# Kernel tuning notes

Measured on AMD Instinct MI355X. Metric: run time of the kernel, lower is better.

The kernel has to match this reference:

```python
import jax, jax.numpy as jnp
import numpy as np
import math

E = 512
W = 16


def overlap_and_add(signal, frame_step):
    """signal: [..., frames, frame_length] -> [..., frame_step*(frames-1)+frame_length]."""
    outer = signal.shape[:-2]
    frames, frame_length = signal.shape[-2:]
    subframe_length = math.gcd(frame_length, frame_step)
    subframe_step = frame_step // subframe_length
    subframes_per_frame = frame_length // subframe_length
    output_size = frame_step * (frames - 1) + frame_length
    output_subframes = output_size // subframe_length

    # [B, frames*subframes_per_frame, subframe_length]
    B = int(np.prod(outer)) if outer else 1
    sub = signal.reshape(B, frames * subframes_per_frame, subframe_length)
    # destination subframe index for each source subframe
    idx = (jnp.arange(frames)[:, None] * subframe_step
           + jnp.arange(subframes_per_frame)[None, :]).reshape(-1)
    out = jnp.zeros((B, output_subframes, subframe_length), signal.dtype)
    out = out.at[:, idx, :].add(sub)
    return out.reshape(*outer, output_size)


def setup_inputs() -> dict:
    key = jax.random.key(0)
    k1, k2 = jax.random.split(key)
    mixture_w = jax.random.normal(k1, (8, 2, 16000, E), dtype=jnp.float32)
    # nn.Linear(E, W).weight has shape [W, E]
    basis_weight = jax.random.normal(k2, (W, E), dtype=jnp.float32) * (1.0 / math.sqrt(E))
    return {"mixture_w": mixture_w, "basis_weight": basis_weight}


def reference(mixture_w, basis_weight):
    # est_source: [..., frames, W]
    est_source = jnp.einsum('bckE,wE->bckw', mixture_w, basis_weight)
    return overlap_and_add(est_source, W // 2)
```

## Files before the change

### kernel.cpp

```cpp
#include <hip/hip_runtime.h>


#define FRAMES 16000
#define EDIM   512
#define OUTF   16001
#define OUT_PER_BC 128008
#define BATCHES 16
#define OFPW    128

__global__ __launch_bounds__(128, 2)
void decoder_kernel(const float* __restrict__ A,
                    const float* __restrict__ B,
                    float* __restrict__ out)
{
    const int t   = threadIdx.x;
    const int wid = t >> 6;
    const int l   = t & 63;
    const int wq  = l & 7;
    const int ksl = l >> 3;
    const int bc  = blockIdx.y;
    const int o0  = (blockIdx.x * 2 + wid) * OFPW;

    __shared__ float ring[2][16][16];

    const float4* B4 = (const float4*)B;
    float4 Bw[2][2][8];
    #pragma unroll
    for (int w = 0; w < 2; ++w)
        #pragma unroll
        for (int h = 0; h < 2; ++h)
            #pragma unroll
            for (int j = 0; j < 8; ++j)
                Bw[w][h][j] = B4[(2*wq + w) * 128 + ksl*16 + h*8 + j];

    const float4* Abc = (const float4*)(A + (size_t)bc * FRAMES * EDIM);

    float4 Abuf[2][8];

    auto loadHalf = [&](float4* dst, int f, int h) {
        int fc = f; if (fc < 0) fc = 0; if (fc >= FRAMES) fc = FRAMES - 1;
        const float4* p = Abc + (size_t)fc * 128 + ksl*16 + h*8;
        #pragma unroll
        for (int j = 0; j < 8; ++j) dst[j] = p[j];
    };

    auto processFrame = [&](int f) {
        loadHalf(Abuf[1], f, 1);
        float acc[2][2] = {{0.f,0.f},{0.f,0.f}};
        #pragma unroll
        for (int j = 0; j < 8; ++j) {
            const float4 a = Abuf[0][j];
            acc[0][0] = fmaf(a.x, Bw[0][0][j].x, acc[0][0]);
            acc[0][0] = fmaf(a.y, Bw[0][0][j].y, acc[0][0]);
            acc[0][0] = fmaf(a.z, Bw[0][0][j].z, acc[0][0]);
            acc[0][0] = fmaf(a.w, Bw[0][0][j].w, acc[0][0]);
            acc[1][0] = fmaf(a.x, Bw[1][0][j].x, acc[1][0]);
            acc[1][0] = fmaf(a.y, Bw[1][0][j].y, acc[1][0]);
            acc[1][0] = fmaf(a.z, Bw[1][0][j].z, acc[1][0]);
            acc[1][0] = fmaf(a.w, Bw[1][0][j].w, acc[1][0]);
        }
        loadHalf(Abuf[0], f + 1, 0);
        #pragma unroll
        for (int j = 0; j < 8; ++j) {
            const float4 a = Abuf[1][j];
            acc[0][1] = fmaf(a.x, Bw[0][1][j].x, acc[0][1]);
            acc[0][1] = fmaf(a.y, Bw[0][1][j].y, acc[0][1]);
            acc[0][1] = fmaf(a.z, Bw[0][1][j].z, acc[0][1]);
            acc[0][1] = fmaf(a.w, Bw[0][1][j].w, acc[0][1]);
            acc[1][1] = fmaf(a.x, Bw[1][1][j].x, acc[1][1]);
            acc[1][1] = fmaf(a.y, Bw[1][1][j].y, acc[1][1]);
            acc[1][1] = fmaf(a.z, Bw[1][1][j].z, acc[1][1]);
            acc[1][1] = fmaf(a.w, Bw[1][1][j].w, acc[1][1]);
        }
        float r0 = acc[0][0] + acc[0][1];
        float r1 = acc[1][0] + acc[1][1];
        r0 += __shfl_xor(r0, 8);   r1 += __shfl_xor(r1, 8);
        r0 += __shfl_xor(r0, 16);  r1 += __shfl_xor(r1, 16);
        r0 += __shfl_xor(r0, 32);  r1 += __shfl_xor(r1, 32);
        if (f < 0 || f >= FRAMES) { r0 = 0.f; r1 = 0.f; }
        if (ksl == 0) {
            *(float2*)&ring[wid][f & 15][2*wq] = make_float2(r0, r1);
        }
    };

    loadHalf(Abuf[0], o0 - 1, 0);
    processFrame(o0 - 1);

    for (int b = 0; b < BATCHES; ++b) {
        const int cf = o0 + b * 8;
        #pragma unroll
        for (int r = 0; r < 8; ++r) processFrame(cf + r);
        __syncthreads();
        const int fr = cf + (l >> 3);
        const float v = ring[wid][fr & 15][l & 7]
                      + ring[wid][(fr - 1) & 15][8 + (l & 7)];
        if (fr < OUTF)
            out[(size_t)bc * OUT_PER_BC + (size_t)cf * 8 + l] = v;
    }
}

extern "C" void kernel_launch(void* const* d_in, const int* in_sizes, int n_in,
                              void* d_out, int out_size, void* d_ws, size_t ws_size,
                              hipStream_t stream) {
    const float* A   = (const float*)d_in[0];
    const float* B   = (const float*)d_in[1];
    float*       out = (float*)d_out;

    dim3 grid(63, 16, 1);
    decoder_kernel<<<grid, dim3(128, 1, 1), 0, stream>>>(A, B, out);
}
```

Baseline: 745.9 us.

## Replace LDS ring with shuffle-based overlap-add and deeper quarter-frame load pipeline

Each block is now a single wavefront, and the shared-memory ring plus __syncthreads is removed. Overlap-add is done with cross-lane shuffles, combining the current frame's first half with the previous frame's second half. Loads are split into quarter-frame chunks and rotated through a 6-slot register ring, so global loads are issued several steps ahead of the FMAs that use them. The goal is to hide memory latency in this bandwidth-bound kernel and drop the barrier. In exchange there are more shuffles per frame, narrower 8-lane output stores, and more register pressure.

```diff
diff --git a/kernel.cpp b/kernel.cpp
--- a/kernel.cpp
+++ b/kernel.cpp
@@ -2,101 +2,100 @@
 
 
 #define FRAMES 16000
-#define EDIM   512
 #define OUTF   16001
 #define OUT_PER_BC 128008
-#define BATCHES 16
-#define OFPW    128
+#define OFPW   128
 
-__global__ __launch_bounds__(128, 2)
+__global__ __launch_bounds__(64, 2)
 void decoder_kernel(const float* __restrict__ A,
                     const float* __restrict__ B,
                     float* __restrict__ out)
 {
-    const int t   = threadIdx.x;
-    const int wid = t >> 6;
-    const int l   = t & 63;
+    const int l   = threadIdx.x & 63;
     const int wq  = l & 7;
     const int ksl = l >> 3;
     const int bc  = blockIdx.y;
-    const int o0  = (blockIdx.x * 2 + wid) * OFPW;
-
-    __shared__ float ring[2][16][16];
+    const int o0  = blockIdx.x * OFPW;
 
     const float4* B4 = (const float4*)B;
-    float4 Bw[2][2][8];
+    float4 Bw[2][16];
     #pragma unroll
     for (int w = 0; w < 2; ++w)
         #pragma unroll
-        for (int h = 0; h < 2; ++h)
-            #pragma unroll
-            for (int j = 0; j < 8; ++j)
-                Bw[w][h][j] = B4[(2*wq + w) * 128 + ksl*16 + h*8 + j];
+        for (int k = 0; k < 16; ++k)
+            Bw[w][k] = B4[(2*wq + w) * 128 + ksl*16 + k];
 
-    const float4* Abc = (const float4*)(A + (size_t)bc * FRAMES * EDIM);
+    const float4* Abc = (const float4*)A + (size_t)bc * FRAMES * 128;
 
-    float4 Abuf[2][8];
+    float4 ring[6][4];
+    float acc0 = 0.f, acc1 = 0.f;
+    float prev0 = 0.f, prev1 = 0.f;
 
-    auto loadHalf = [&](float4* dst, int f, int h) {
-        int fc = f; if (fc < 0) fc = 0; if (fc >= FRAMES) fc = FRAMES - 1;
-        const float4* p = Abc + (size_t)fc * 128 + ksl*16 + h*8;
-        #pragma unroll
-        for (int j = 0; j < 8; ++j) dst[j] = p[j];
-    };
+#define LOADQ(SLOT, FIDX, Q) do {                                         \
+        int fc_ = o0 - 1 + (FIDX);                                        \
+        fc_ = fc_ < 0 ? 0 : (fc_ >= FRAMES ? FRAMES - 1 : fc_);           \
+        const float4* p_ = Abc + (size_t)fc_ * 128 + ksl * 16 + (Q) * 4;  \
+        ring[SLOT][0] = p_[0]; ring[SLOT][1] = p_[1];                     \
+        ring[SLOT][2] = p_[2]; ring[SLOT][3] = p_[3];                     \
+    } while (0)
 
-    auto processFrame = [&](int f) {
-        loadHalf(Abuf[1], f, 1);
-        float acc[2][2] = {{0.f,0.f},{0.f,0.f}};
-        #pragma unroll
-        for (int j = 0; j < 8; ++j) {
-            const float4 a = Abuf[0][j];
-            acc[0][0] = fmaf(a.x, Bw[0][0][j].x, acc[0][0]);
-            acc[0][0] = fmaf(a.y, Bw[0][0][j].y, acc[0][0]);
-            acc[0][0] = fmaf(a.z, Bw[0][0][j].z, acc[0][0]);
-            acc[0][0] = fmaf(a.w, Bw[0][0][j].w, acc[0][0]);
-            acc[1][0] = fmaf(a.x, Bw[1][0][j].x, acc[1][0]);
-            acc[1][0] = fmaf(a.y, Bw[1][0][j].y, acc[1][0]);
-            acc[1][0] = fmaf(a.z, Bw[1][0][j].z, acc[1][0]);
-            acc[1][0] = fmaf(a.w, Bw[1][0][j].w, acc[1][0]);
-        }
-        loadHalf(Abuf[0], f + 1, 0);
-        #pragma unroll
-        for (int j = 0; j < 8; ++j) {
-            const float4 a = Abuf[1][j];
-            acc[0][1] = fmaf(a.x, Bw[0][1][j].x, acc[0][1]);
-            acc[0][1] = fmaf(a.y, Bw[0][1][j].y, acc[0][1]);
-            acc[0][1] = fmaf(a.z, Bw[0][1][j].z, acc[0][1]);
-            acc[0][1] = fmaf(a.w, Bw[0][1][j].w, acc[0][1]);
-            acc[1][1] = fmaf(a.x, Bw[1][1][j].x, acc[1][1]);
-            acc[1][1] = fmaf(a.y, Bw[1][1][j].y, acc[1][1]);
-            acc[1][1] = fmaf(a.z, Bw[1][1][j].z, acc[1][1]);
-            acc[1][1] = fmaf(a.w, Bw[1][1][j].w, acc[1][1]);
-        }
-        float r0 = acc[0][0] + acc[0][1];
-        float r1 = acc[1][0] + acc[1][1];
+#define COMPQ(SLOT, Q) do {                                                   \
+        _Pragma("unroll")                                                     \
+        for (int j_ = 0; j_ < 4; ++j_) {                                      \
+            const float4 a_  = ring[SLOT][j_];                                \
+            const float4 b0_ = Bw[0][(Q)*4 + j_];                             \
+            const float4 b1_ = Bw[1][(Q)*4 + j_];                             \
+            acc0 = fmaf(a_.x, b0_.x, acc0); acc1 = fmaf(a_.x, b1_.x, acc1);   \
+            acc0 = fmaf(a_.y, b0_.y, acc0); acc1 = fmaf(a_.y, b1_.y, acc1);   \
+            acc0 = fmaf(a_.z, b0_.z, acc0); acc1 = fmaf(a_.z, b1_.z, acc1);   \
+            acc0 = fmaf(a_.w, b0_.w, acc0); acc1 = fmaf(a_.w, b1_.w, acc1);   \
+        }                                                                     \
+    } while (0)
+
+    auto frameEnd = [&](int fidx) {
+        float r0 = acc0, r1 = acc1;
         r0 += __shfl_xor(r0, 8);   r1 += __shfl_xor(r1, 8);
         r0 += __shfl_xor(r0, 16);  r1 += __shfl_xor(r1, 16);
         r0 += __shfl_xor(r0, 32);  r1 += __shfl_xor(r1, 32);
+        const int f = o0 - 1 + fidx;
         if (f < 0 || f >= FRAMES) { r0 = 0.f; r1 = 0.f; }
-        if (ksl == 0) {
-            *(float2*)&ring[wid][f & 15][2*wq] = make_float2(r0, r1);
+        if (fidx >= 1 && f < OUTF) {
+            const int srcA = (l & 56) | (wq >> 1);
+            const float xa0 = __shfl(r0, srcA);
+            const float xa1 = __shfl(r1, srcA);
+            const int srcB = srcA | 4;
+            const float yb0 = __shfl(prev0, srcB);
+            const float yb1 = __shfl(prev1, srcB);
+            const float av = (wq & 1) ? xa1 : xa0;
+            const float bv = (wq & 1) ? yb1 : yb0;
+            if (ksl == 0)
+                out[(size_t)bc * OUT_PER_BC + (size_t)f * 8 + wq] = av + bv;
         }
+        prev0 = r0; prev1 = r1;
+        acc0 = 0.f; acc1 = 0.f;
     };
 
-    loadHalf(Abuf[0], o0 - 1, 0);
-    processFrame(o0 - 1);
+    LOADQ(0, 0, 0); LOADQ(1, 0, 1); LOADQ(2, 0, 2); LOADQ(3, 0, 3);
+    LOADQ(4, 1, 0);
 
-    for (int b = 0; b < BATCHES; ++b) {
-        const int cf = o0 + b * 8;
-        #pragma unroll
-        for (int r = 0; r < 8; ++r) processFrame(cf + r);
-        __syncthreads();
-        const int fr = cf + (l >> 3);
-        const float v = ring[wid][fr & 15][l & 7]
-                      + ring[wid][(fr - 1) & 15][8 + (l & 7)];
-        if (fr < OUTF)
-            out[(size_t)bc * OUT_PER_BC + (size_t)cf * 8 + l] = v;
+    for (int t = 0; t < 43; ++t) {
+        const int fb = 3 * t;
+        LOADQ(5, fb + 1, 1); COMPQ(0, 0);
+        LOADQ(0, fb + 1, 2); COMPQ(1, 1);
+        LOADQ(1, fb + 1, 3); COMPQ(2, 2);
+        LOADQ(2, fb + 2, 0); COMPQ(3, 3); frameEnd(fb + 0);
+        LOADQ(3, fb + 2, 1); COMPQ(4, 0);
+        LOADQ(4, fb + 2, 2); COMPQ(5, 1);
+        LOADQ(5, fb + 2, 3); COMPQ(0, 2);
+        LOADQ(0, fb + 3, 0); COMPQ(1, 3); frameEnd(fb + 1);
+        LOADQ(1, fb + 3, 1); COMPQ(2, 0);
+        LOADQ(2, fb + 3, 2); COMPQ(3, 1);
+        LOADQ(3, fb + 3, 3); COMPQ(4, 2);
+        LOADQ(4, fb + 4, 0); COMPQ(5, 3); frameEnd(fb + 2);
     }
+
+#undef LOADQ
+#undef COMPQ
 }
 
 extern "C" void kernel_launch(void* const* d_in, const int* in_sizes, int n_in,
@@ -106,6 +105,6 @@
     const float* B   = (const float*)d_in[1];
     float*       out = (float*)d_out;
 
-    dim3 grid(63, 16, 1);
-    decoder_kernel<<<grid, dim3(128, 1, 1), 0, stream>>>(A, B, out);
+    dim3 grid(126, 16, 1);
+    decoder_kernel<<<grid, dim3(64, 1, 1), 0, stream>>>(A, B, out);
 }
```

Measured after the change: 761.0 us. +2.0%, slower.
